# Kernel optimization log

Hardware: AMD Instinct MI355X
Metric: run time of the kernel (lower is better)

The kernel has to match this reference:

```python
import jax, jax.numpy as jnp
import numpy as np


def conv1x1(x, w, bias):
    # x: [B,C,H,W], w: [O,C], bias: [O]
    return jnp.einsum('bchw,oc->bohw', x, w) + bias[None, :, None, None]


def setup_inputs() -> dict:
    key = jax.random.key(0)
    ks = jax.random.split(key, 12)
    B, Cin_half, H, W = 8, 128, 128, 128
    Cin, Cout = 256, 256
    s_in = 1.0 / np.sqrt(Cin)
    s_out = 1.0 / np.sqrt(Cout)
    return {
        'a': jax.random.normal(ks[0], (B, Cin_half, H, W), jnp.float32),
        'b': jax.random.normal(ks[1], (B, Cin_half, H, W), jnp.float32),
        'w1': jax.random.uniform(ks[2], (Cout, Cin), jnp.float32, -s_in, s_in),
        'b1': jax.random.uniform(ks[3], (Cout,), jnp.float32, -s_in, s_in),
        'w2': jax.random.uniform(ks[4], (Cout, Cout), jnp.float32, -s_out, s_out),
        'b2': jax.random.uniform(ks[5], (Cout,), jnp.float32, -s_out, s_out),
        'w3': jax.random.uniform(ks[6], (Cout, Cout), jnp.float32, -s_out, s_out),
        'b3': jax.random.uniform(ks[7], (Cout,), jnp.float32, -s_out, s_out),
        'w4': jax.random.uniform(ks[8], (Cout, Cout), jnp.float32, -s_out, s_out),
        'b4': jax.random.uniform(ks[9], (Cout,), jnp.float32, -s_out, s_out),
    }


def reference(a, b, w1, b1, w2, b2, w3, b3, w4, b4):
    z = jnp.concatenate([a, b], axis=1)            # [B, Cin, H, W]
    z = conv1x1(z, w1, b1)                          # [B, C, H, W]
    B, C, H, W = z.shape
    q = conv1x1(z, w2, b2).reshape(B, C, H * W)     # [B, C, N]
    k = conv1x1(z, w3, b3).reshape(B, C, H * W)
    v = conv1x1(z, w4, b4).reshape(B, C, H * W)
    qk = jnp.einsum('bcn,bdn->bcd', q, k)           # [B, C, C] (q @ k^T)
    attn = jax.nn.softmax(qk, axis=-1)
    out = jnp.einsum('bcd,bdn->bcn', attn, v)       # [B, C, N]
    return out.reshape(B, C, H, W)
```

## Files before the change

kernel.cpp:

```cpp
#include <hip/hip_runtime.h>

typedef float  f4v  __attribute__((ext_vector_type(4)));
typedef __bf16 bf8v __attribute__((ext_vector_type(8)));
typedef unsigned int u32x2 __attribute__((ext_vector_type(2)));
typedef unsigned int u32x4 __attribute__((ext_vector_type(4)));
typedef unsigned short u16;
typedef unsigned short u16x8 __attribute__((ext_vector_type(8)));

#define MFMA(a,b,c) __builtin_amdgcn_mfma_f32_16x16x32_bf16((a),(b),(c),0,0,0)
#define HW_N 16384

__device__ __forceinline__ u16 bf_rne(float x){
  unsigned u = __float_as_uint(x);
  u += 0x7fffu + ((u >> 16) & 1u);
  return (u16)(u >> 16);
}

__global__ void k_weights(const float* __restrict__ w1, const float* __restrict__ b1,
                          const float* __restrict__ w2, const float* __restrict__ b2,
                          const float* __restrict__ w3, const float* __restrict__ b3,
                          const float* __restrict__ w4, const float* __restrict__ b4,
                          float* __restrict__ Wq, float* __restrict__ WkT,
                          float* __restrict__ Wv, float* __restrict__ bq,
                          float* __restrict__ bk, float* __restrict__ bv)
{
  const int blk = blockIdx.x, t = threadIdx.x;
  if (blk == 96){
    float aq = 0.f, ak = 0.f, av = 0.f;
    for (int j = 0; j < 256; ++j){
      const float bb = b1[j];
      aq += w2[t*256 + j] * bb;
      ak += w3[t*256 + j] * bb;
      av += w4[t*256 + j] * bb;
    }
    bq[t] = aq + b2[t];
    bk[t] = ak + b3[t];
    bv[t] = av + b4[t];
    return;
  }
  for (int i = 0; i < 8; ++i){
    const int e   = blk*2048 + i*256 + t;
    const int mat = e >> 16;
    const int c   = (e >> 8) & 255;
    const int col = e & 255;
    const float* wsrc = (mat == 0) ? w2 : ((mat == 1) ? w3 : w4);
    float acc = 0.f;
    for (int j = 0; j < 256; ++j) acc += wsrc[c*256 + j] * w1[j*256 + col];
    if      (mat == 0) Wq [c*256 + col] = acc;
    else if (mat == 1) WkT[col*256 + c] = acc;
    else               Wv [c*256 + col] = acc;
  }
}

__global__ __launch_bounds__(512, 2) void k_gram(
    const float* __restrict__ xa, const float* __restrict__ xb,
    float* __restrict__ G, float* __restrict__ spart,
    u16* __restrict__ xbf)
{
  __shared__ u16 hbuf[2][256*64];
  __shared__ u16 lbuf[2][256*64];
  const int blk = blockIdx.x;
  const int b = blk >> 5, half = (blk >> 4) & 1, chunk = blk & 15;
  const int t = threadIdx.x;
  const int lane = t & 63, w = t >> 6;
  const int wr = w >> 1, wc = w & 1;
  const int c4 = t & 15, crow = t >> 4;

  const float* rowp[8];
#pragma unroll
  for (int p = 0; p < 8; ++p){
    const int c = crow + 32*p;
    const float* base = (c < 128) ? (xa + (size_t)(b*128 + c) * HW_N)
                                  : (xb + (size_t)(b*128 + (c-128)) * HW_N);
    rowp[p] = base + c4*4;
  }

  float ssum[8];
#pragma unroll
  for (int p = 0; p < 8; ++p) ssum[p] = 0.f;

  const f4v vzero = {0.f, 0.f, 0.f, 0.f};
  f4v acc[4][4];
#pragma unroll
  for (int i = 0; i < 4; ++i)
#pragma unroll
    for (int j = 0; j < 4; ++j) acc[i][j] = vzero;

  f4v ld[8];
  auto issue = [&](int s){
    const int n0 = chunk*1024 + s*64;
#pragma unroll
    for (int p = 0; p < 8; ++p) ld[p] = *(const f4v*)(rowp[p] + n0);
  };
  auto wbuf = [&](int bi, int s){
#pragma unroll
    for (int p = 0; p < 8; ++p){
      const int c = crow + 32*p;
      const f4v v = ld[p];
      ssum[p] += (v[0] + v[1]) + (v[2] + v[3]);
      u16 h[4], l[4];
#pragma unroll
      for (int i = 0; i < 4; ++i){
        const float x = v[i];
        const u16 hb = bf_rne(x);
        const float hf = __uint_as_float(((unsigned)hb) << 16);
        h[i] = hb; l[i] = bf_rne(x - hf);
      }
      u32x2 hp, lp;
      hp[0] = (unsigned)h[0] | ((unsigned)h[1] << 16);
      hp[1] = (unsigned)h[2] | ((unsigned)h[3] << 16);
      lp[0] = (unsigned)l[0] | ((unsigned)l[1] << 16);
      lp[1] = (unsigned)l[2] | ((unsigned)l[3] << 16);
      const int off = c*64 + (((c4 >> 1) ^ (c & 7)) * 8) + (c4 & 1) * 4;
      *(u32x2*)&hbuf[bi][off] = hp;
      *(u32x2*)&lbuf[bi][off] = lp;
      if (half == 0){
        *(u32x2*)&xbf[(size_t)(b*256 + c)*HW_N + chunk*1024 + s*64 + c4*4] = hp;
      }
    }
  };
  auto mstep = [&](int bi){
#pragma unroll
    for (int kk = 0; kk < 2; ++kk){
      bf8v ah[4], al[4], bh[4], bl[4];
#pragma unroll
      for (int f = 0; f < 4; ++f){
        const int so = kk*4 + (lane >> 4);
        const int r  = wr*64 + f*16 + (lane & 15);
        const int oa = r*64 + ((so ^ (r & 7)) * 8);
        ah[f] = *(const bf8v*)&hbuf[bi][oa];
        al[f] = *(const bf8v*)&lbuf[bi][oa];
        const int rc = 128*half + wc*64 + f*16 + (lane & 15);
        const int ob = rc*64 + ((so ^ (rc & 7)) * 8);
        bh[f] = *(const bf8v*)&hbuf[bi][ob];
        bl[f] = *(const bf8v*)&lbuf[bi][ob];
      }
#pragma unroll
      for (int i = 0; i < 4; ++i)
#pragma unroll
        for (int j = 0; j < 4; ++j){
          acc[i][j] = MFMA(ah[i], bh[j], acc[i][j]);
          acc[i][j] = MFMA(ah[i], bl[j], acc[i][j]);
          acc[i][j] = MFMA(al[i], bh[j], acc[i][j]);
        }
    }
  };

  issue(0); wbuf(0, 0); __syncthreads();
  for (int s = 0; s < 16; ++s){
    const int cur = s & 1;
    if (s < 15) issue(s + 1);
    mstep(cur);
    if (s < 15) wbuf(cur ^ 1, s + 1);
    __syncthreads();
  }

  float* gb = G + (size_t)b * 65536;
#pragma unroll
  for (int i = 0; i < 4; ++i)
#pragma unroll
    for (int j = 0; j < 4; ++j){
      const int row = wr*64 + i*16 + ((lane >> 4) << 2);
      const int col = 128*half + wc*64 + j*16 + (lane & 15);
#pragma unroll
      for (int r2 = 0; r2 < 4; ++r2)
        atomicAdd(&gb[(size_t)(row + r2)*256 + col], acc[i][j][r2]);
    }

  if (half == 0){
#pragma unroll
    for (int p = 0; p < 8; ++p){
      float v = ssum[p];
      v += __shfl_xor(v, 1);
      v += __shfl_xor(v, 2);
      v += __shfl_xor(v, 4);
      v += __shfl_xor(v, 8);
      if ((lane & 15) == 0)
        spart[(b*16 + chunk)*256 + (crow + 32*p)] = v;
    }
  }
}

__device__ __forceinline__ float block_red(float v, int ismax, volatile float* red, int t){
#pragma unroll
  for (int m = 32; m; m >>= 1){
    const float o = __shfl_xor(v, m);
    v = ismax ? fmaxf(v, o) : (v + o);
  }
  if ((t & 63) == 0) red[t >> 6] = v;
  __syncthreads();
  const float r01 = ismax ? fmaxf(red[0], red[1]) : (red[0] + red[1]);
  const float r23 = ismax ? fmaxf(red[2], red[3]) : (red[2] + red[3]);
  v = ismax ? fmaxf(r01, r23) : (r01 + r23);
  __syncthreads();
  return v;
}

__global__ __launch_bounds__(256, 2) void k_attn(
    const float* __restrict__ G, const float* __restrict__ spart,
    const float* __restrict__ Wq, const float* __restrict__ WkT,
    const float* __restrict__ Wv, const float* __restrict__ bq,
    const float* __restrict__ bk, const float* __restrict__ bv,
    u16* __restrict__ Mfrag, float* __restrict__ cb)
{
  __shared__ float s_lds[256];
  __shared__ float wq_lds[4][256];
  __shared__ float t1_lds[4][256];
  __shared__ float a_lds[4][256];
  __shared__ float red[4];
  const int blk = blockIdx.x;
  const int b = blk >> 6, r0 = (blk & 63) * 4;
  const int t = threadIdx.x;

  float sv = 0.f;
#pragma unroll
  for (int ch = 0; ch < 16; ++ch) sv += spart[(b*16 + ch)*256 + t];
  s_lds[t] = sv;
#pragma unroll
  for (int ri = 0; ri < 4; ++ri) wq_lds[ri][t] = Wq[(r0 + ri)*256 + t];
  __syncthreads();

  float t1[4] = {0,0,0,0}, pv[4] = {0,0,0,0};
  const float* gb = G + (size_t)b * 65536;
  for (int k = 0; k < 256; ++k){
    const float g  = gb[k*256 + t];
    const float sk = s_lds[k];
#pragma unroll
    for (int ri = 0; ri < 4; ++ri){
      const float wqv = wq_lds[ri][k];
      t1[ri] += wqv * g;
      pv[ri] += wqv * sk;
    }
  }
#pragma unroll
  for (int ri = 0; ri < 4; ++ri) t1_lds[ri][t] = t1[ri];
  __syncthreads();

  float qk[4] = {0,0,0,0}, rd = 0.f;
  for (int n = 0; n < 256; ++n){
    const float wkt = WkT[n*256 + t];
    rd += wkt * s_lds[n];
#pragma unroll
    for (int ri = 0; ri < 4; ++ri) qk[ri] += t1_lds[ri][n] * wkt;
  }
  const float bkv = bk[t];
#pragma unroll
  for (int ri = 0; ri < 4; ++ri){
    const float bqv = bq[r0 + ri];
    qk[ri] += pv[ri]*bkv + bqv*rd + 16384.f*bqv*bkv;
  }

  float areg[4];
#pragma unroll
  for (int ri = 0; ri < 4; ++ri){
    const float m = block_red(qk[ri], 1, red, t);
    const float e = __expf(qk[ri] - m);
    const float s = block_red(e, 0, red, t);
    areg[ri] = e / s;
    a_lds[ri][t] = areg[ri];
  }
  const float bvv = bv[t];
#pragma unroll
  for (int ri = 0; ri < 4; ++ri){
    const float c = block_red(areg[ri]*bvv, 0, red, t);
    if (t == 0) cb[b*256 + r0 + ri] = c;
  }
  __syncthreads();

  float m4[4] = {0,0,0,0};
  for (int d = 0; d < 256; ++d){
    const float wv = Wv[d*256 + t];
#pragma unroll
    for (int ri = 0; ri < 4; ++ri) m4[ri] += a_lds[ri][d] * wv;
  }
  const int ks = t >> 5, lhi = (t >> 3) & 3, j = t & 7;
#pragma unroll
  for (int ri = 0; ri < 4; ++ri){
    const int o = r0 + ri;
    Mfrag[(size_t)b*65536 +
          (size_t)((((o >> 4)*8 + ks)*64) + (o & 15) + (lhi << 4))*8 + j] = bf_rne(m4[ri]);
  }
}

__global__ __launch_bounds__(512, 4) void k_out(
    const u16* __restrict__ xbf, const u16* __restrict__ Mfrag,
    const float* __restrict__ cb, float* __restrict__ out)
{
  __shared__ u16 xt[2][32*256];
  const int blk = blockIdx.x;
  const int b = blk >> 6, nchunk = blk & 63;
  const int t = threadIdx.x;
  const int lane = t & 63, w = t >> 6;
  const int cr = t >> 1;
  const int hf = t & 1;

  const u16* xp = xbf + (((size_t)(b*256) + cr) << 14) + nchunk*256 + hf*16;

  u16x8 ld[2];
  auto issue = [&](int s){
#pragma unroll
    for (int q = 0; q < 2; ++q) ld[q] = *(const u16x8*)(xp + s*32 + q*8);
  };
  auto swrite = [&](int bi){
#pragma unroll
    for (int q = 0; q < 2; ++q){
#pragma unroll
      for (int j = 0; j < 8; ++j){
        const int n = hf*16 + q*8 + j;
        xt[bi][n*256 + (((cr >> 3) ^ (n & 15))*8) + (cr & 7)] = ld[q][j];
      }
    }
  };

  issue(0);

  u32x4 af[2][8];
  const u16* mb = Mfrag + (size_t)b * 65536;
#pragma unroll
  for (int f = 0; f < 2; ++f)
#pragma unroll
    for (int ks = 0; ks < 8; ++ks)
      af[f][ks] = *(const u32x4*)(mb + (size_t)((((w*2 + f)*8 + ks)*64 + lane))*8);
#pragma unroll
  for (int f = 0; f < 2; ++f)
#pragma unroll
    for (int ks = 0; ks < 8; ++ks)
      asm volatile("" : "+a"(af[f][ks]));

  float cbv[2];
#pragma unroll
  for (int f = 0; f < 2; ++f)
    cbv[f] = cb[b*256 + w*32 + f*16 + (lane & 15)];

  const f4v vzero = {0.f, 0.f, 0.f, 0.f};
  float* outp = out + (size_t)b*256*HW_N;

  swrite(0);
  __syncthreads();

  for (int s = 0; s < 8; ++s){
    const int cur = s & 1;
    if (s < 7) issue(s + 1);

    const int n0 = nchunk*256 + s*32;
    f4v acc[2][2];
#pragma unroll
    for (int f = 0; f < 2; ++f){ acc[f][0] = vzero; acc[f][1] = vzero; }

#pragma unroll
    for (int ks = 0; ks < 8; ++ks){
      bf8v xf[2];
#pragma unroll
      for (int g = 0; g < 2; ++g){
        const int n  = g*16 + (lane & 15);
        const int so = ks*4 + (lane >> 4);
        xf[g] = *(const bf8v*)&xt[cur][n*256 + ((so ^ (n & 15))*8)];
      }
#pragma unroll
      for (int f = 0; f < 2; ++f){
        acc[f][0] = MFMA(xf[0], __builtin_bit_cast(bf8v, af[f][ks]), acc[f][0]);
        acc[f][1] = MFMA(xf[1], __builtin_bit_cast(bf8v, af[f][ks]), acc[f][1]);
      }
    }

#pragma unroll
    for (int f = 0; f < 2; ++f){
      const int row = w*32 + f*16 + (lane & 15);
#pragma unroll
      for (int g = 0; g < 2; ++g){
        const int px = n0 + g*16 + ((lane >> 4) << 2);
        f4v v = acc[f][g] + cbv[f];
        *(f4v*)&outp[(size_t)row*HW_N + px] = v;
      }
    }

    if (s < 7) swrite(cur ^ 1);
    __syncthreads();
  }
}

extern "C" void kernel_launch(void* const* d_in, const int* in_sizes, int n_in,
                              void* d_out, int out_size, void* d_ws, size_t ws_size,
                              hipStream_t stream)
{
  const float* xa = (const float*)d_in[0];
  const float* xb = (const float*)d_in[1];
  const float* w1 = (const float*)d_in[2];
  const float* b1 = (const float*)d_in[3];
  const float* w2 = (const float*)d_in[4];
  const float* b2 = (const float*)d_in[5];
  const float* w3 = (const float*)d_in[6];
  const float* b3 = (const float*)d_in[7];
  const float* w4 = (const float*)d_in[8];
  const float* b4 = (const float*)d_in[9];
  float* out = (float*)d_out;
  char*  ws  = (char*)d_ws;

  float* G     = (float*)(ws + 0);
  float* spart = (float*)(ws + 2097152);
  float* Wq    = (float*)(ws + 2228224);
  float* WkT   = (float*)(ws + 2490368);
  float* Wv    = (float*)(ws + 2752512);
  float* bq    = (float*)(ws + 3014656);
  float* bk    = (float*)(ws + 3015680);
  float* bv    = (float*)(ws + 3016704);
  u16*   Mfrag = (u16*)  (ws + 3017728);
  float* cb    = (float*)(ws + 4066304);
  u16*   xbf   = (u16*)  (ws + 4074496);

  hipMemsetAsync(G, 0, 2097152, stream);
  hipLaunchKernelGGL(k_weights, dim3(97),  dim3(256), 0, stream,
                     w1,b1,w2,b2,w3,b3,w4,b4, Wq,WkT,Wv,bq,bk,bv);
  hipLaunchKernelGGL(k_gram,    dim3(256), dim3(512), 0, stream,
                     xa, xb, G, spart, xbf);
  hipLaunchKernelGGL(k_attn,    dim3(512), dim3(256), 0, stream,
                     G, spart, Wq, WkT, Wv, bq, bk, bv, Mfrag, cb);
  hipLaunchKernelGGL(k_out,     dim3(512), dim3(512), 0, stream,
                     xbf, Mfrag, cb, out);
}
```

Measured before the change: 288.1 us.

## Drop bf16 x staging buffer; read fp32 input directly in output kernel

The gram kernel no longer writes a bf16 copy of the input to workspace. The output kernel instead reads the fp32 inputs directly and converts them to bf16 while staging into shared memory. The gram kernel also drops its double-buffered LDS in favour of single buffers with an extra barrier, and raises its launch bounds to 4 blocks per CU to allow more occupancy. This removes a 64 MB write and replaces a 64 MB bf16 read with a 128 MB fp32 read, trading global traffic for lost load/compute overlap in the gram loop.

Result: slower. 357.6 us (+24.1%).

```diff
diff --git a/kernel.cpp b/kernel.cpp
--- a/kernel.cpp
+++ b/kernel.cpp
@@ -5,7 +5,6 @@
 typedef unsigned int u32x2 __attribute__((ext_vector_type(2)));
 typedef unsigned int u32x4 __attribute__((ext_vector_type(4)));
 typedef unsigned short u16;
-typedef unsigned short u16x8 __attribute__((ext_vector_type(8)));
 
 #define MFMA(a,b,c) __builtin_amdgcn_mfma_f32_16x16x32_bf16((a),(b),(c),0,0,0)
 #define HW_N 16384
@@ -52,13 +51,12 @@
   }
 }
 
-__global__ __launch_bounds__(512, 2) void k_gram(
+__global__ __launch_bounds__(512, 4) void k_gram(
     const float* __restrict__ xa, const float* __restrict__ xb,
-    float* __restrict__ G, float* __restrict__ spart,
-    u16* __restrict__ xbf)
+    float* __restrict__ G, float* __restrict__ spart)
 {
-  __shared__ u16 hbuf[2][256*64];
-  __shared__ u16 lbuf[2][256*64];
+  __shared__ u16 hbuf[256*64];
+  __shared__ u16 lbuf[256*64];
   const int blk = blockIdx.x;
   const int b = blk >> 5, half = (blk >> 4) & 1, chunk = blk & 15;
   const int t = threadIdx.x;
@@ -92,7 +90,7 @@
 #pragma unroll
     for (int p = 0; p < 8; ++p) ld[p] = *(const f4v*)(rowp[p] + n0);
   };
-  auto wbuf = [&](int bi, int s){
+  auto wbuf = [&](){
 #pragma unroll
     for (int p = 0; p < 8; ++p){
       const int c = crow + 32*p;
@@ -112,14 +110,11 @@
       lp[0] = (unsigned)l[0] | ((unsigned)l[1] << 16);
       lp[1] = (unsigned)l[2] | ((unsigned)l[3] << 16);
       const int off = c*64 + (((c4 >> 1) ^ (c & 7)) * 8) + (c4 & 1) * 4;
-      *(u32x2*)&hbuf[bi][off] = hp;
-      *(u32x2*)&lbuf[bi][off] = lp;
-      if (half == 0){
-        *(u32x2*)&xbf[(size_t)(b*256 + c)*HW_N + chunk*1024 + s*64 + c4*4] = hp;
-      }
+      *(u32x2*)&hbuf[off] = hp;
+      *(u32x2*)&lbuf[off] = lp;
     }
   };
-  auto mstep = [&](int bi){
+  auto mstep = [&](){
 #pragma unroll
     for (int kk = 0; kk < 2; ++kk){
       bf8v ah[4], al[4], bh[4], bl[4];
@@ -128,12 +123,12 @@
         const int so = kk*4 + (lane >> 4);
         const int r  = wr*64 + f*16 + (lane & 15);
         const int oa = r*64 + ((so ^ (r & 7)) * 8);
-        ah[f] = *(const bf8v*)&hbuf[bi][oa];
-        al[f] = *(const bf8v*)&lbuf[bi][oa];
+        ah[f] = *(const bf8v*)&hbuf[oa];
+        al[f] = *(const bf8v*)&lbuf[oa];
         const int rc = 128*half + wc*64 + f*16 + (lane & 15);
         const int ob = rc*64 + ((so ^ (rc & 7)) * 8);
-        bh[f] = *(const bf8v*)&hbuf[bi][ob];
-        bl[f] = *(const bf8v*)&lbuf[bi][ob];
+        bh[f] = *(const bf8v*)&hbuf[ob];
+        bl[f] = *(const bf8v*)&lbuf[ob];
       }
 #pragma unroll
       for (int i = 0; i < 4; ++i)
@@ -146,13 +141,15 @@
     }
   };
 
-  issue(0); wbuf(0, 0); __syncthreads();
+  issue(0); wbuf(); __syncthreads();
   for (int s = 0; s < 16; ++s){
-    const int cur = s & 1;
     if (s < 15) issue(s + 1);
-    mstep(cur);
-    if (s < 15) wbuf(cur ^ 1, s + 1);
+    mstep();
     __syncthreads();
+    if (s < 15){
+      wbuf();
+      __syncthreads();
+    }
   }
 
   float* gb = G + (size_t)b * 65536;
@@ -283,8 +280,9 @@
 }
 
 __global__ __launch_bounds__(512, 4) void k_out(
-    const u16* __restrict__ xbf, const u16* __restrict__ Mfrag,
-    const float* __restrict__ cb, float* __restrict__ out)
+    const float* __restrict__ xa, const float* __restrict__ xb,
+    const u16* __restrict__ Mfrag, const float* __restrict__ cb,
+    float* __restrict__ out)
 {
   __shared__ u16 xt[2][32*256];
   const int blk = blockIdx.x;
@@ -294,20 +292,24 @@
   const int cr = t >> 1;
   const int hf = t & 1;
 
-  const u16* xp = xbf + (((size_t)(b*256) + cr) << 14) + nchunk*256 + hf*16;
-
-  u16x8 ld[2];
+  const float* rowbase = (cr < 128) ? (xa + (size_t)(b*128 + cr)*HW_N)
+                                    : (xb + (size_t)(b*128 + (cr-128))*HW_N);
+  const float* rp = rowbase + hf*16;
+
+  f4v ld[4];
   auto issue = [&](int s){
-#pragma unroll
-    for (int q = 0; q < 2; ++q) ld[q] = *(const u16x8*)(xp + s*32 + q*8);
+    const int n0 = nchunk*256 + s*32;
+#pragma unroll
+    for (int q = 0; q < 4; ++q) ld[q] = *(const f4v*)(rp + n0 + q*4);
   };
-  auto swrite = [&](int bi){
-#pragma unroll
-    for (int q = 0; q < 2; ++q){
-#pragma unroll
-      for (int j = 0; j < 8; ++j){
-        const int n = hf*16 + q*8 + j;
-        xt[bi][n*256 + (((cr >> 3) ^ (n & 15))*8) + (cr & 7)] = ld[q][j];
+  auto cvtwrite = [&](int bi){
+#pragma unroll
+    for (int q = 0; q < 4; ++q){
+      const f4v v = ld[q];
+#pragma unroll
+      for (int i = 0; i < 4; ++i){
+        const int n = hf*16 + q*4 + i;
+        xt[bi][n*256 + (((cr >> 3) ^ (n & 15))*8) + (cr & 7)] = bf_rne(v[i]);
       }
     }
   };
@@ -335,7 +337,7 @@
   const f4v vzero = {0.f, 0.f, 0.f, 0.f};
   float* outp = out + (size_t)b*256*HW_N;
 
-  swrite(0);
+  cvtwrite(0);
   __syncthreads();
 
   for (int s = 0; s < 8; ++s){
@@ -374,7 +376,7 @@
       }
     }
 
-    if (s < 7) swrite(cur ^ 1);
+    if (s < 7) cvtwrite(cur ^ 1);
     __syncthreads();
   }
 }
@@ -406,15 +408,14 @@
   float* bv    = (float*)(ws + 3016704);
   u16*   Mfrag = (u16*)  (ws + 3017728);
   float* cb    = (float*)(ws + 4066304);
-  u16*   xbf   = (u16*)  (ws + 4074496);
 
   hipMemsetAsync(G, 0, 2097152, stream);
   hipLaunchKernelGGL(k_weights, dim3(97),  dim3(256), 0, stream,
                      w1,b1,w2,b2,w3,b3,w4,b4, Wq,WkT,Wv,bq,bk,bv);
   hipLaunchKernelGGL(k_gram,    dim3(256), dim3(512), 0, stream,
-                     xa, xb, G, spart, xbf);
+                     xa, xb, G, spart);
   hipLaunchKernelGGL(k_attn,    dim3(512), dim3(256), 0, stream,
                      G, spart, Wq, WkT, Wv, bq, bk, bv, Mfrag, cb);
   hipLaunchKernelGGL(k_out,     dim3(512), dim3(512), 0, stream,
-                     xbf, Mfrag, cb, out);
-}
+                     xa, xb, Mfrag, cb, out);
+}
```
